# Kernel optimization log

Measured on AMD Instinct MI355X. Metric: run time of the kernel, lower is better.

Reference implementation:

```python
import jax, jax.numpy as jnp
import numpy as np

B, NPG, DEG = 256, 128, 16          # graphs per side, nodes per graph, avg degree
N = B * NPG                          # 32768 nodes per side
E = N * DEG                          # 524288 edges per side
F_IN, F1, F2, F3 = 64, 128, 64, 32   # number_labels, filters_1..3
TN, BINS = 16, 16                    # tensor_neurons, bins


def setup_inputs() -> dict:
    key = jax.random.key(0)
    ks = jax.random.split(key, 24)

    def make_edges(k):
        # random edges, each constrained within its own graph block
        base = jax.random.randint(k, (2, E), 0, NPG)
        off = jnp.repeat(jnp.arange(B, dtype=jnp.int64) * NPG, NPG * DEG)
        return (base + off[None, :]).astype(jnp.int64)

    def w(k, shape, fan_in):
        return (jax.random.normal(k, shape, jnp.float32) / np.sqrt(fan_in)).astype(jnp.float32)

    batch = jnp.repeat(jnp.arange(B, dtype=jnp.int64), NPG)
    return {
        'x1': jax.random.normal(ks[0], (N, F_IN), jnp.float32),
        'edge_index_1': make_edges(ks[1]),
        'batch_1': batch,
        'x2': jax.random.normal(ks[2], (N, F_IN), jnp.float32),
        'edge_index_2': make_edges(ks[3]),
        'batch_2': batch,
        # GCN layer params
        'W1': w(ks[4], (F_IN, F1), F_IN), 'b1': jnp.zeros((F1,), jnp.float32),
        'W2': w(ks[5], (F1, F2), F1),     'b2': jnp.zeros((F2,), jnp.float32),
        'W3': w(ks[6], (F2, F3), F2),     'b3': jnp.zeros((F3,), jnp.float32),
        # attention pooling
        'attW': w(ks[7], (F3, F3), F3),
        # tensor network module
        'tW': w(ks[8], (F3, F3, TN), F3),
        'tblock': w(ks[9], (TN, 2 * F3), 2 * F3),
        'tbias': jnp.zeros((TN,), jnp.float32),
        # scoring MLP (feature_count = TN + BINS -> 16 -> 1)
        'sW1': w(ks[10], (TN + BINS, 16), TN + BINS), 'sb1': jnp.zeros((16,), jnp.float32),
        'sW2': w(ks[11], (16, 1), 16),                'sb2': jnp.zeros((1,), jnp.float32),
    }


def _gcn(x, W, b, src, dst):
    # PyG GCNConv: add self-loops, symmetric deg^-1/2 normalization, then scatter-add
    n = x.shape[0]
    loop = jnp.arange(n, dtype=src.dtype)
    s = jnp.concatenate([src, loop])
    d = jnp.concatenate([dst, loop])
    deg = jax.ops.segment_sum(jnp.ones_like(d, dtype=x.dtype), d, num_segments=n)
    dinv = jax.lax.rsqrt(jnp.maximum(deg, 1e-12))
    norm = dinv[s] * dinv[d]                      # [E+N]
    h = x @ W                                     # [N, Fout]
    out = jax.ops.segment_sum(norm[:, None] * h[s], d, num_segments=n)
    return out + b


def _histc(v):
    # torch.histc with bins=BINS, min=max=0 -> uses data min/max; last bin inclusive
    v = v.reshape(-1)
    lo, hi = v.min(), v.max()
    idx = jnp.floor((v - lo) / jnp.maximum(hi - lo, 1e-12) * BINS)
    idx = jnp.clip(idx, 0, BINS - 1).astype(jnp.int32)
    h = jax.ops.segment_sum(jnp.ones_like(v), idx, num_segments=BINS)
    return h / h.sum()


def reference(x1, edge_index_1, batch_1, x2, edge_index_2, batch_2,
              W1, b1, W2, b2, W3, b3, attW, tW, tblock, tbias,
              sW1, sb1, sW2, sb2):
    def conv_pass(x, ei):
        src, dst = ei[0], ei[1]
        h = jax.nn.relu(_gcn(x, W1, b1, src, dst))   # dropout inactive (eval)
        h = jax.nn.relu(_gcn(h, W2, b2, src, dst))
        return _gcn(h, W3, b3, src, dst)

    f1 = conv_pass(x1, edge_index_1)
    f2 = conv_pass(x2, edge_index_2)

    # to_dense_batch: equal-sized, batch-sorted graphs -> plain reshape, full masks
    d1 = f1.reshape(B, NPG, F3)
    d2 = f2.reshape(B, NPG, F3)

    # per-graph-pair similarity histogram (detached in original)
    scores = jnp.einsum('bnd,bmd->bnm', jax.lax.stop_gradient(d1), jax.lax.stop_gradient(d2))
    hist = jax.vmap(_histc)(jax.nn.sigmoid(scores))  # [B, BINS]

    # attention pooling (SimGNN AttentionModule)
    def attn_pool(d):
        ctx = jnp.tanh(jnp.mean(d @ attW, axis=1))             # [B, F3]
        att = jax.nn.sigmoid(jnp.einsum('bnd,bd->bn', d, ctx))  # [B, NPG]
        return jnp.einsum('bnd,bn->bd', d, att)                 # [B, F3]

    e1 = attn_pool(d1)
    e2 = attn_pool(d2)

    # tensor network scoring
    tensor_scores = jnp.einsum('bi,ijk,bj->bk', e1, tW, e2)
    block_scores = jnp.concatenate([e1, e2], axis=-1) @ tblock.T
    tnm = jax.nn.relu(tensor_scores + block_scores + tbias)      # [B, TN]

    feat = jnp.concatenate([tnm, hist], axis=1)                  # [B, TN+BINS]
    h = jax.nn.relu(feat @ sW1 + sb1)
    score = jax.nn.sigmoid(h @ sW2 + sb2)
    return score.squeeze(-1)                                     # [B]
```

## Files before the change

kernel.cpp:

```cpp
#include <hip/hip_runtime.h>
#include <hip/hip_bf16.h>
#include <hip/hip_fp16.h>

#define N_NODES 32768
#define N_EDGES 524288
#define NGRAPH  256
#define NPG     128
#define EPG     2048
#define F_IN    64
#define F1      128
#define F2      64
#define F3      32
#define TN      16
#define BINS    16

typedef _Float16 f16;
typedef _Float16 f16x4 __attribute__((ext_vector_type(4)));
typedef _Float16 f16x8 __attribute__((ext_vector_type(8)));
typedef float    f32x4 __attribute__((ext_vector_type(4)));

__device__ __forceinline__ float sigmoidf(float x) { return 1.f / (1.f + expf(-x)); }

#define L_A    0
#define L_R1   34816
#define L_R2   69632
#define L_R3   88064
#define L_R4   106496
#define L_R5   123904
#define L_DT   128512
#define L_DINV 148992
#define POOLB  149504

#define SA  136
#define SB  72
#define SD  40

template<int N, int K, int AS, int BS, int OS, bool TRANS, bool RELU>
__device__ __forceinline__ void mfma_mm(const f16* __restrict__ A,
                                        const f16* __restrict__ B,
                                        const float* __restrict__ bias,
                                        f16* __restrict__ out, int tid) {
    const int w = tid >> 6, lane = tid & 63;
    const int col = lane & 15, g = lane >> 4;
    const int strip = w & 7, nh = w >> 3;
    const int rowa = strip * 16 + col;
    constexpr int NT = N / 16, KS = K / 32, NT2 = NT / 2;
    f32x4 acc[NT2];
#pragma unroll
    for (int nt = 0; nt < NT2; ++nt) {
        const float b = bias ? bias[(nh * NT2 + nt) * 16 + col] : 0.f;
        acc[nt] = (f32x4){b, b, b, b};
    }
#pragma unroll
    for (int ks = 0; ks < KS; ++ks) {
        const f16x8 a = *(const f16x8*)&A[rowa * AS + ks * 32 + g * 8];
#pragma unroll
        for (int nt = 0; nt < NT2; ++nt) {
            const f16x8 b = *(const f16x8*)&B[((nh * NT2 + nt) * 16 + col) * BS + ks * 32 + g * 8];
            acc[nt] = __builtin_amdgcn_mfma_f32_16x16x32_f16(a, b, acc[nt], 0, 0, 0);
        }
    }
#pragma unroll
    for (int nt = 0; nt < NT2; ++nt) {
        const int c = (nh * NT2 + nt) * 16 + col;
        if (TRANS) {
            f16x4 o;
#pragma unroll
            for (int j = 0; j < 4; ++j) {
                float v = acc[nt][j];
                if (RELU) v = fmaxf(v, 0.f);
                o[j] = (f16)v;
            }
            *(f16x4*)&out[c * OS + strip * 16 + g * 4] = o;
        } else {
#pragma unroll
            for (int j = 0; j < 4; ++j) {
                float v = acc[nt][j];
                if (RELU) v = fmaxf(v, 0.f);
                out[(strip * 16 + g * 4 + j) * OS + c] = (f16)v;
            }
        }
    }
}

__global__ __launch_bounds__(1024, 4) void genn_all(
    const float* __restrict__ x1, const int* __restrict__ ei1,
    const float* __restrict__ x2, const int* __restrict__ ei2,
    const float* __restrict__ W1, const float* __restrict__ b1,
    const float* __restrict__ W2, const float* __restrict__ b2,
    const float* __restrict__ W3, const float* __restrict__ b3,
    const float* __restrict__ attW, const float* __restrict__ tW,
    const float* __restrict__ tblk, const float* __restrict__ tbias,
    const float* __restrict__ sW1, const float* __restrict__ sb1,
    const float* __restrict__ sW2, const float* __restrict__ sb2,
    float* __restrict__ outp) {
    __shared__ __align__(16) char pool[POOLB];
    unsigned int* Acnt = (unsigned int*)(pool + L_A);
    f16*   Amat = (f16*)(pool + L_A);
    f16*   dts  = (f16*)(pool + L_DT);
    float* dinv = (float*)(pool + L_DINV);

    const int g = blockIdx.x;
    const int tid = threadIdx.x;
    const int wv = tid >> 6, lane = tid & 63;

    for (int side = 0; side < 2; ++side) {
        const float* xg = (side ? x2 : x1) + (size_t)g * NPG * F_IN;
        const int* eib  = side ? ei2 : ei1;
        const int* srcg = eib + (size_t)g * EPG;
        const int* dstg = eib + N_EDGES + (size_t)g * EPG;
        const int nb = g * NPG;

        for (int i = tid; i < 2176; i += 1024)
            ((uint4*)Acnt)[i] = make_uint4(0, 0, 0, 0);
        __syncthreads();

#pragma unroll
        for (int it = 0; it < EPG / 1024; ++it) {
            const int e = it * 1024 + tid;
            const int d = dstg[e] - nb;
            const int s = srcg[e] - nb;
            atomicAdd(&Acnt[d * 68 + (s >> 1)], 1u << ((s & 1) << 4));
        }
        {
            f16* xT = (f16*)(pool + L_R1);
#pragma unroll
            for (int it = 0; it < 2; ++it) {
                const int idx = (it * 1024 + tid) * 4;
                const float4 v = *(const float4*)&xg[idx];
                const int n = idx >> 6, c = idx & 63;
                xT[(c + 0) * SA + n] = (f16)v.x;
                xT[(c + 1) * SA + n] = (f16)v.y;
                xT[(c + 2) * SA + n] = (f16)v.z;
                xT[(c + 3) * SA + n] = (f16)v.w;
            }
            f16* W1T = (f16*)(pool + L_R2);
            for (int i = tid; i < F_IN * F1; i += 1024)
                W1T[(i & 127) * SB + (i >> 7)] = (f16)W1[i];
            if (side == 0) {
                f16* W2T = (f16*)(pool + L_R4);
                for (int i = tid; i < F1 * F2; i += 1024)
                    W2T[(i & 63) * SA + (i >> 6)] = (f16)W2[i];
                f16* W3T = (f16*)(pool + L_R5);
                for (int i = tid; i < F2 * F3; i += 1024)
                    W3T[(i & 31) * SB + (i >> 5)] = (f16)W3[i];
            }
        }
        __syncthreads();

        if (tid < 512) {
            const int d = tid >> 2, q = tid & 3;
            unsigned int s = 0;
            const unsigned int* rp = &Acnt[d * 68 + q * 17];
            for (int j = 0; j < 17; ++j) {
                const unsigned int v = rp[j];
                s += (v & 0xffffu) + (v >> 16);
            }
            s += __shfl_down((int)s, 2);
            s += __shfl_down((int)s, 1);
            if (q == 0) dinv[d] = rsqrtf((float)s + 1.0f);
        }
        __syncthreads();

        for (int i = tid; i < 8704; i += 1024) {
            const int d = i / 68, w = i % 68;
            const unsigned int v = Acnt[i];
            const int s0 = 2 * w, s1 = 2 * w + 1;
            int c0 = v & 0xffffu, c1 = v >> 16;
            if (s0 == d) ++c0;
            if (s1 == d) ++c1;
            const float dd = dinv[d];
            const f16 f0 = (f16)((float)c0 * dinv[s0 & 127] * dd);
            const f16 f1 = (f16)((float)c1 * dinv[s1 & 127] * dd);
            unsigned short u0 = __builtin_bit_cast(unsigned short, f0);
            unsigned short u1 = __builtin_bit_cast(unsigned short, f1);
            Acnt[i] = (unsigned int)u0 | ((unsigned int)u1 << 16);
        }
        __syncthreads();

        f16* xT   = (f16*)(pool + L_R1);
        f16* h1   = (f16*)(pool + L_R1);
        f16* W1T  = (f16*)(pool + L_R2);
        f16* h2   = (f16*)(pool + L_R2);
        f16* out1 = (f16*)(pool + L_R3);
        f16* t2T  = (f16*)(pool + L_R3);
        f16* t3T  = (f16*)(pool + L_R3);
        f16* W2T  = (f16*)(pool + L_R4);
        f16* W3T  = (f16*)(pool + L_R5);

        mfma_mm<64, 128, SA, SA, SB, false, false>(Amat, xT, nullptr, out1, tid);
        __syncthreads();
        mfma_mm<128, 64, SB, SB, SA, false, true>(out1, W1T, b1, h1, tid);
        __syncthreads();
        mfma_mm<64, 128, SA, SA, SA, true, false>(h1, W2T, nullptr, t2T, tid);
        __syncthreads();
        mfma_mm<64, 128, SA, SA, SB, false, true>(Amat, t2T, b2, h2, tid);
        __syncthreads();
        mfma_mm<32, 64, SB, SB, SA, true, false>(h2, W3T, nullptr, t3T, tid);
        __syncthreads();
        mfma_mm<32, 128, SA, SA, SD, false, false>(Amat, t3T, b3,
                                                   dts + side * (NPG * SD), tid);
        __syncthreads();
    }

    unsigned char* lhist = (unsigned char*)(pool + L_R4);
    float* pf   = (float*)(pool + L_R3);
    float* red  = pf;
    float* lohi = pf + 32;
    float* meanv= pf + 34;
    float* ctxv = pf + 98;
    float* ev   = pf + 162;
    float* feat = pf + 226;
    float* hv   = pf + 258;
    float* thr  = pf + 274;
    float* av   = pf + 290;
    float* pmean= pf + 546;
    float* ptens= pf + 1570;
    int*   bins2= (int*)(pf + 2082);
    const f16* d1 = dts;
    const f16* d2 = dts + NPG * SD;

    const int col = lane & 15, gq = lane >> 4;
    const int strip = wv & 7, nh = wv >> 3;
    const int rowa = strip * 16 + col;
    f32x4 acc[4];
#pragma unroll
    for (int nt = 0; nt < 4; ++nt) acc[nt] = (f32x4){0.f, 0.f, 0.f, 0.f};
    {
        const f16x8 a = *(const f16x8*)&d1[rowa * SD + gq * 8];
#pragma unroll
        for (int nt = 0; nt < 4; ++nt) {
            const f16x8 b = *(const f16x8*)&d2[((nh * 4 + nt) * 16 + col) * SD + gq * 8];
            acc[nt] = __builtin_amdgcn_mfma_f32_16x16x32_f16(a, b, acc[nt], 0, 0, 0);
        }
    }
    for (int i = tid; i < 4352; i += 1024) ((unsigned int*)lhist)[i] = 0u;
    float lmin = acc[0][0], lmax = acc[0][0];
#pragma unroll
    for (int nt = 0; nt < 4; ++nt)
#pragma unroll
        for (int j = 0; j < 4; ++j) {
            lmin = fminf(lmin, acc[nt][j]);
            lmax = fmaxf(lmax, acc[nt][j]);
        }
    for (int off = 32; off; off >>= 1) {
        lmin = fminf(lmin, __shfl_down(lmin, off));
        lmax = fmaxf(lmax, __shfl_down(lmax, off));
    }
    if (lane == 0) { red[wv] = lmin; red[16 + wv] = lmax; }
    __syncthreads();
    if (tid == 0) {
        float mn = red[0], mx = red[16];
        for (int w = 1; w < 16; ++w) { mn = fminf(mn, red[w]); mx = fmaxf(mx, red[16 + w]); }
        const float los = sigmoidf(mn);
        const float den = fmaxf(sigmoidf(mx) - los, 1e-12f);
        lohi[0] = los;
        lohi[1] = den;
    }
    __syncthreads();
    if (tid < 15) {
        const float p = lohi[0] + (float)(tid + 1) * lohi[1] * (1.f / 16.f);
        thr[tid] = logf(p / (1.f - p));
    }
    __syncthreads();

    {
        unsigned char* lh = &lhist[tid * 17];
#pragma unroll
        for (int nt = 0; nt < 4; ++nt)
#pragma unroll
            for (int j = 0; j < 4; ++j) {
                const float x = acc[nt][j];
                int b = 0;
#pragma unroll
                for (int k = 0; k < 15; ++k) b += (x >= thr[k]) ? 1 : 0;
                lh[b]++;
            }
    }
    __syncthreads();
    if (tid < 256) {
        const int b = tid & 15, chunk = tid >> 4;
        int s = 0;
        for (int i = 0; i < 64; ++i) s += lhist[(chunk * 64 + i) * 17 + b];
        bins2[chunk * 16 + b] = s;
    }
    __syncthreads();

    {
        const int cc = tid & 63, chunk = tid >> 6;
        const int side = cc >> 5, c = cc & 31;
        const f16* dp = dts + side * (NPG * SD);
        float s = 0.f;
        const int nbs = chunk * 8;
        for (int n = 0; n < 8; ++n) s += (float)dp[(nbs + n) * SD + c];
        pmean[chunk * 64 + cc] = s;
    }
    __syncthreads();
    if (tid < 64) {
        float s = 0.f;
        for (int c = 0; c < 16; ++c) s += pmean[c * 64 + tid];
        meanv[tid] = s * (1.f / NPG);
    }
    __syncthreads();
    if (tid < 64) {
        const int c = tid & 31;
        const float* mv = &meanv[(tid >> 5) * 32];
        float a = 0.f;
        for (int k = 0; k < F3; ++k) a += mv[k] * attW[k * F3 + c];
        ctxv[tid] = tanhf(a);
    }
    __syncthreads();
    if (tid < 256) {
        const int n = tid & 127, side = tid >> 7;
        const f16* dp = dts + side * (NPG * SD);
        const float* cx = &ctxv[side * 32];
        float a = 0.f;
        for (int k = 0; k < F3; ++k) a += (float)dp[n * SD + k] * cx[k];
        av[tid] = sigmoidf(a);
    }
    __syncthreads();
    {
        const int cc = tid & 63, chunk = tid >> 6;
        const int side = cc >> 5, c = cc & 31;
        const f16* dp = dts + side * (NPG * SD);
        const float* a = &av[side * 128];
        float s = 0.f;
        const int nbs = chunk * 8;
        for (int n = 0; n < 8; ++n) s += a[nbs + n] * (float)dp[(nbs + n) * SD + c];
        pmean[chunk * 64 + cc] = s;
    }
    __syncthreads();
    if (tid < 64) {
        float s = 0.f;
        for (int c = 0; c < 16; ++c) s += pmean[c * 64 + tid];
        ev[tid] = s;
    }
    __syncthreads();

    if (tid < 512) {
        const int k = tid & 15, i = tid >> 4;
        const float e1i = ev[i];
        float a = 0.f;
        for (int j = 0; j < F3; ++j) a += ev[32 + j] * tW[(i * F3 + j) * TN + k];
        ptens[i * 16 + k] = e1i * a;
    }
    __syncthreads();
    if (tid < TN) {
        float a = tbias[tid];
        for (int i = 0; i < 32; ++i) a += ptens[i * 16 + tid];
        for (int i = 0; i < F3; ++i) a += ev[i] * tblk[tid * 2 * F3 + i];
        for (int j = 0; j < F3; ++j) a += ev[32 + j] * tblk[tid * 2 * F3 + F3 + j];
        feat[tid] = fmaxf(a, 0.f);
    } else if (tid < TN + BINS) {
        const int b = tid - TN;
        int s = 0;
        for (int c = 0; c < 16; ++c) s += bins2[c * 16 + b];
        feat[tid] = (float)s * (1.f / (NPG * NPG));
    }
    __syncthreads();
    if (tid < 16) {
        float a = sb1[tid];
        for (int i = 0; i < TN + BINS; ++i) a += feat[i] * sW1[i * 16 + tid];
        hv[tid] = fmaxf(a, 0.f);
    }
    __syncthreads();
    if (tid == 0) {
        float a = sb2[0];
        for (int j = 0; j < 16; ++j) a += hv[j] * sW2[j];
        outp[g] = sigmoidf(a);
    }
}

extern "C" void kernel_launch(void* const* d_in, const int* in_sizes, int n_in,
                              void* d_out, int out_size, void* d_ws, size_t ws_size,
                              hipStream_t stream) {
    const float* x1   = (const float*)d_in[0];
    const int*   ei1  = (const int*)d_in[1];
    const float* x2   = (const float*)d_in[3];
    const int*   ei2  = (const int*)d_in[4];
    const float* W1   = (const float*)d_in[6];
    const float* b1   = (const float*)d_in[7];
    const float* W2   = (const float*)d_in[8];
    const float* b2   = (const float*)d_in[9];
    const float* W3   = (const float*)d_in[10];
    const float* b3   = (const float*)d_in[11];
    const float* attW = (const float*)d_in[12];
    const float* tW   = (const float*)d_in[13];
    const float* tblk = (const float*)d_in[14];
    const float* tbias= (const float*)d_in[15];
    const float* sW1  = (const float*)d_in[16];
    const float* sb1  = (const float*)d_in[17];
    const float* sW2  = (const float*)d_in[18];
    const float* sb2  = (const float*)d_in[19];
    float* out = (float*)d_out;
    (void)in_sizes; (void)n_in; (void)out_size; (void)d_ws; (void)ws_size;

    genn_all<<<NGRAPH, 1024, 0, stream>>>(x1, ei1, x2, ei2,
                                          W1, b1, W2, b2, W3, b3,
                                          attW, tW, tblk, tbias,
                                          sW1, sb1, sW2, sb2, out);
}
```

Measured before the change: 34.87 us.

## Compute histogram bins directly and transpose per-thread histogram layout

Replaces the 15-threshold logit comparison loop with a direct bin index computed from sigmoid and a precomputed scale, removing one barrier and the threshold setup step. The per-thread byte histograms are stored bin-major with a padded stride, so the reduction reads them as 16-byte vectors instead of strided bytes. W1 is now converted only once, on side 0, and h2 is moved to region R1 so the transposed W1 is not overwritten. Direct binning can place values near bin edges differently from the threshold method because of rounding.

```diff
diff --git a/kernel.cpp b/kernel.cpp
--- a/kernel.cpp
+++ b/kernel.cpp
@@ -34,6 +34,7 @@
 #define SA  136
 #define SB  72
 #define SD  40
+#define LHS 1040
 
 template<int N, int K, int AS, int BS, int OS, bool TRANS, bool RELU>
 __device__ __forceinline__ void mfma_mm(const f16* __restrict__ A,
@@ -134,10 +135,10 @@
                 xT[(c + 2) * SA + n] = (f16)v.z;
                 xT[(c + 3) * SA + n] = (f16)v.w;
             }
-            f16* W1T = (f16*)(pool + L_R2);
-            for (int i = tid; i < F_IN * F1; i += 1024)
-                W1T[(i & 127) * SB + (i >> 7)] = (f16)W1[i];
             if (side == 0) {
+                f16* W1T = (f16*)(pool + L_R2);
+                for (int i = tid; i < F_IN * F1; i += 1024)
+                    W1T[(i & 127) * SB + (i >> 7)] = (f16)W1[i];
                 f16* W2T = (f16*)(pool + L_R4);
                 for (int i = tid; i < F1 * F2; i += 1024)
                     W2T[(i & 63) * SA + (i >> 6)] = (f16)W2[i];
@@ -180,8 +181,8 @@
 
         f16* xT   = (f16*)(pool + L_R1);
         f16* h1   = (f16*)(pool + L_R1);
+        f16* h2   = (f16*)(pool + L_R1);
         f16* W1T  = (f16*)(pool + L_R2);
-        f16* h2   = (f16*)(pool + L_R2);
         f16* out1 = (f16*)(pool + L_R3);
         f16* t2T  = (f16*)(pool + L_R3);
         f16* t3T  = (f16*)(pool + L_R3);
@@ -212,7 +213,6 @@
     float* ev   = pf + 162;
     float* feat = pf + 226;
     float* hv   = pf + 258;
-    float* thr  = pf + 274;
     float* av   = pf + 290;
     float* pmean= pf + 546;
     float* ptens= pf + 1570;
@@ -234,7 +234,7 @@
             acc[nt] = __builtin_amdgcn_mfma_f32_16x16x32_f16(a, b, acc[nt], 0, 0, 0);
         }
     }
-    for (int i = tid; i < 4352; i += 1024) ((unsigned int*)lhist)[i] = 0u;
+    for (int i = tid; i < 17 * LHS / 4; i += 1024) ((unsigned int*)lhist)[i] = 0u;
     float lmin = acc[0][0], lmax = acc[0][0];
 #pragma unroll
     for (int nt = 0; nt < 4; ++nt)
@@ -255,33 +255,37 @@
         const float los = sigmoidf(mn);
         const float den = fmaxf(sigmoidf(mx) - los, 1e-12f);
         lohi[0] = los;
-        lohi[1] = den;
-    }
-    __syncthreads();
-    if (tid < 15) {
-        const float p = lohi[0] + (float)(tid + 1) * lohi[1] * (1.f / 16.f);
-        thr[tid] = logf(p / (1.f - p));
+        lohi[1] = (float)BINS / den;
     }
     __syncthreads();
 
     {
-        unsigned char* lh = &lhist[tid * 17];
+        const float lo = lohi[0], sc = lohi[1];
+        unsigned char* lh = lhist + tid;
 #pragma unroll
         for (int nt = 0; nt < 4; ++nt)
 #pragma unroll
             for (int j = 0; j < 4; ++j) {
-                const float x = acc[nt][j];
-                int b = 0;
-#pragma unroll
-                for (int k = 0; k < 15; ++k) b += (x >= thr[k]) ? 1 : 0;
-                lh[b]++;
+                const float v = sigmoidf(acc[nt][j]);
+                int b = (int)((v - lo) * sc);
+                b = min(max(b, 0), BINS - 1);
+                lh[b * LHS]++;
             }
     }
     __syncthreads();
     if (tid < 256) {
         const int b = tid & 15, chunk = tid >> 4;
+        const unsigned char* row = lhist + b * LHS + chunk * 64;
         int s = 0;
-        for (int i = 0; i < 64; ++i) s += lhist[(chunk * 64 + i) * 17 + b];
+#pragma unroll
+        for (int i = 0; i < 4; ++i) {
+            const uint4 v = *(const uint4*)(row + i * 16);
+            unsigned int u;
+            u = v.x; s += (u & 255) + ((u >> 8) & 255) + ((u >> 16) & 255) + (u >> 24);
+            u = v.y; s += (u & 255) + ((u >> 8) & 255) + ((u >> 16) & 255) + (u >> 24);
+            u = v.z; s += (u & 255) + ((u >> 8) & 255) + ((u >> 16) & 255) + (u >> 24);
+            u = v.w; s += (u & 255) + ((u >> 8) & 255) + ((u >> 16) & 255) + (u >> 24);
+        }
         bins2[chunk * 16 + b] = s;
     }
     __syncthreads();
```

Result: faster. 33.29 us (-4.5%).
